# Optimization experiments

Hardware: AMD Instinct MI355X
Metric: run time of the kernel (lower is better)

## Reference

```python
import jax, jax.numpy as jnp
import numpy as np

B, D, H, O, E, TOP_K = 1024, 1024, 2048, 1024, 8, 2


def setup_inputs() -> dict:
    key = jax.random.key(0)
    ks = jax.random.split(key, 8)
    s = 0.02
    return {
        "x":  jax.random.normal(ks[0], (B, D), dtype=jnp.float32),
        "Wr": jax.random.normal(ks[1], (D, E), dtype=jnp.float32) * s,
        "br": jnp.zeros((E,), dtype=jnp.float32),
        "W1": jax.random.normal(ks[2], (E, D, H), dtype=jnp.float32) * s,
        "b1": jnp.zeros((E, H), dtype=jnp.float32),
        "W2": jax.random.normal(ks[3], (E, H, H), dtype=jnp.float32) * s,
        "b2": jnp.zeros((E, H), dtype=jnp.float32),
        "W3": jax.random.normal(ks[4], (E, H, O), dtype=jnp.float32) * s,
        "b3": jnp.zeros((E, O), dtype=jnp.float32),
    }


def reference(x, Wr, br, W1, b1, W2, b2, W3, b3):
    # --- router: softmax -> top-k -> renormalize selected weights ---
    logits = x @ Wr + br                      # [B, E]
    probs = jax.nn.softmax(logits, axis=-1)
    w, ids = jax.lax.top_k(probs, TOP_K)      # [B, K], [B, K]
    w = w / (jnp.sum(w, axis=-1, keepdims=True) + 1e-6)

    # --- expert MLPs (depth=2: in->h, relu, h->h, relu, h->out) ---
    h = jax.nn.relu(jnp.einsum('bd,edh->beh', x, W1) + b1)   # [B, E, H]
    h = jax.nn.relu(jnp.einsum('beh,ehg->beg', h, W2) + b2)  # [B, E, H]
    y_e = jnp.einsum('beg,ego->beo', h, W3) + b3             # [B, E, O]

    # --- weighted scatter-combine: comb[b,e] = sum_k w[b,k] * [ids[b,k]==e] ---
    comb = jnp.sum(jax.nn.one_hot(ids, E, dtype=x.dtype) * w[..., None], axis=1)  # [B, E]
    out = jnp.einsum('beo,be->bo', y_e, comb)                # [B, O]
    return out
```

## Files before the change

### kernel.cpp

```cpp
#include <hip/hip_runtime.h>
#include <hip/hip_bf16.h>

#define BT 1024
#define DD 1024
#define HH 2048
#define OO 1024
#define EE 8
#define RMAX 3072

typedef __bf16 bf16x8 __attribute__((ext_vector_type(8)));
typedef float  f32x4  __attribute__((ext_vector_type(4)));

__device__ __forceinline__ void cp16(void* l, const void* g) {
    __builtin_amdgcn_global_load_lds(
        (const __attribute__((address_space(1))) void*)g,
        (__attribute__((address_space(3))) void*)l, 16, 0, 0);
}


__global__ __launch_bounds__(256) void router_kernel(
    const float* __restrict__ x, const float* __restrict__ Wr, const float* __restrict__ br,
    int* __restrict__ counts, int* __restrict__ elist,
    int* __restrict__ tok_e, int* __restrict__ tok_p, float* __restrict__ tok_w)
{
    int b = blockIdx.x;
    int tid = threadIdx.x;
    float acc[EE];
#pragma unroll
    for (int e = 0; e < EE; ++e) acc[e] = 0.f;
    const float* xr = x + (size_t)b * DD;
    for (int d = tid; d < DD; d += 256) {
        float xv = xr[d];
#pragma unroll
        for (int e = 0; e < EE; ++e) acc[e] += xv * Wr[d * EE + e];
    }
    __shared__ float red[4][EE];
    int lane = tid & 63, wv = tid >> 6;
#pragma unroll
    for (int e = 0; e < EE; ++e) {
        float v = acc[e];
#pragma unroll
        for (int o = 32; o > 0; o >>= 1) v += __shfl_down(v, o, 64);
        if (lane == 0) red[wv][e] = v;
    }
    __syncthreads();
    if (tid == 0) {
        float lg[EE];
#pragma unroll
        for (int e = 0; e < EE; ++e) lg[e] = red[0][e] + red[1][e] + red[2][e] + red[3][e] + br[e];
        float mx = lg[0];
#pragma unroll
        for (int e = 1; e < EE; ++e) mx = fmaxf(mx, lg[e]);
        float s = 0.f, p[EE];
#pragma unroll
        for (int e = 0; e < EE; ++e) { p[e] = expf(lg[e] - mx); s += p[e]; }
        float inv = 1.f / s;
#pragma unroll
        for (int e = 0; e < EE; ++e) p[e] *= inv;
        int i0 = 0; float b0 = p[0];
#pragma unroll
        for (int e = 1; e < EE; ++e) if (p[e] > b0) { b0 = p[e]; i0 = e; }
        int i1 = -1; float b1v = -1.f;
#pragma unroll
        for (int e = 0; e < EE; ++e) if (e != i0 && p[e] > b1v) { b1v = p[e]; i1 = e; }
        float s2 = b0 + b1v + 1e-6f;
        float w0 = b0 / s2, w1 = b1v / s2;
        int p0 = atomicAdd(&counts[i0], 1);
        int p1 = atomicAdd(&counts[i1], 1);
        elist[i0 * 1024 + p0] = b;
        elist[i1 * 1024 + p1] = b;
        tok_e[2 * b] = i0; tok_e[2 * b + 1] = i1;
        tok_p[2 * b] = p0; tok_p[2 * b + 1] = p1;
        tok_w[2 * b] = w0; tok_w[2 * b + 1] = w1;
    }
}

__global__ void offsets_kernel(const int* __restrict__ counts, int* __restrict__ off)
{
    if (threadIdx.x == 0 && blockIdx.x == 0) {
        int a = 0;
        for (int e = 0; e < EE; ++e) {
            off[e] = a;
            a += ((counts[e] + 127) >> 7) << 7;
        }
        off[EE] = a;
    }
}

__global__ __launch_bounds__(256) void gather_kernel(
    const float* __restrict__ x, const int* __restrict__ counts, const int* __restrict__ off,
    const int* __restrict__ elist, __bf16* __restrict__ Xg)
{
    int e = blockIdx.y;
    int chunk = blockIdx.x >> 2;
    int rg = blockIdx.x & 3;
    int cnt = counts[e];
    if (chunk * 128 >= cnt) return;
    int base = off[e] + chunk * 128 + rg * 32;
    int tid = threadIdx.x;
    for (int it = 0; it < 32; ++it) {
        int slot = chunk * 128 + rg * 32 + it;
        __bf16 v[4];
        if (slot < cnt) {
            int tok = elist[e * 1024 + slot];
            const float4 f = *(const float4*)(x + (size_t)tok * DD + tid * 4);
            v[0] = (__bf16)f.x; v[1] = (__bf16)f.y; v[2] = (__bf16)f.z; v[3] = (__bf16)f.w;
        } else {
            v[0] = v[1] = v[2] = v[3] = (__bf16)0.f;
        }
        *(uint2*)(Xg + (size_t)(base + it) * DD + tid * 4) = *(uint2*)v;
    }
}

template <int K, int N, int TN, bool RELU, bool OUT_BF16>
__global__ __launch_bounds__(256) void gemm_fused(
    const __bf16* __restrict__ A, const float* __restrict__ Wall,
    const float* __restrict__ bias, void* __restrict__ OutV,
    const int* __restrict__ counts, const int* __restrict__ off)
{
    constexpr int NSTEPS = K / 32;
    constexpr int NJ  = TN / 32;
    constexpr int BLD = TN / 8;

    int e  = blockIdx.x & 7;
    int nt = blockIdx.x >> 3;
    int mt = blockIdx.y;
    int cnt = counts[e];
    if (mt * 128 >= cnt) return;
    int row0 = off[e] + mt * 128;

    const __bf16* Ab = A + (size_t)row0 * K;
    const float*  Wp = Wall + (size_t)e * K * N + nt * TN;

    __shared__ __bf16 As[2][128 * 32];
    __shared__ __bf16 Bs[2][TN * 40];

    int tid = threadIdx.x;
    int wave = tid >> 6, lane = tid & 63;
    int m = lane & 15, q = lane >> 4;
    int wm = (wave >> 1) * 64, wn = (wave & 1) * (TN / 2);

    int ar = wave * 16 + (lane >> 2);
    int k8 = (lane & 3) * 8;
    int bn  = (TN == 64) ? (tid & 63) : (tid & 31);
    int bkc = (TN == 64) ? ((tid >> 6) * 8) : ((tid >> 5) * 4);

    float breg[BLD];
    f32x4 acc[4][NJ] = {};

    auto issueA = [&](int t, int buf) {
        const __bf16* src = Ab + t * 32;
        cp16(&As[buf][ar * 32 + k8],        src + (size_t)ar * K + k8);
        cp16(&As[buf][(64 + ar) * 32 + k8], src + (size_t)(64 + ar) * K + k8);
    };
    auto loadB = [&](int t) {
        const float* p = Wp + (size_t)(t * 32 + bkc) * N + bn;
#pragma unroll
        for (int g = 0; g < BLD; ++g) breg[g] = p[(size_t)g * N];
    };
    auto writeB = [&](int buf) {
        __bf16 t8[BLD];
#pragma unroll
        for (int g = 0; g < BLD; ++g) t8[g] = (__bf16)breg[g];
        if constexpr (TN == 64) *(uint4*)(&Bs[buf][bn * 40 + bkc]) = *(uint4*)t8;
        else                    *(uint2*)(&Bs[buf][bn * 40 + bkc]) = *(uint2*)t8;
    };

    issueA(0, 0);
    loadB(0);
    __syncthreads();
    writeB(0);
    __syncthreads();

    for (int t = 0; t < NSTEPS; ++t) {
        int cur = t & 1;
        if (t + 1 < NSTEPS) {
            issueA(t + 1, cur ^ 1);
            loadB(t + 1);
        }
        bf16x8 af[4], bfr[NJ];
#pragma unroll
        for (int i = 0; i < 4; ++i)
            af[i] = *(bf16x8*)(&As[cur][(wm + i * 16 + m) * 32 + q * 8]);
#pragma unroll
        for (int j = 0; j < NJ; ++j)
            bfr[j] = *(bf16x8*)(&Bs[cur][(wn + j * 16 + m) * 40 + q * 8]);
#pragma unroll
        for (int i = 0; i < 4; ++i)
#pragma unroll
            for (int j = 0; j < NJ; ++j)
                acc[i][j] = __builtin_amdgcn_mfma_f32_16x16x32_bf16(af[i], bfr[j], acc[i][j], 0, 0, 0);
        if (t + 1 < NSTEPS) {
            __syncthreads();
            writeB(cur ^ 1);
            __syncthreads();
        }
    }

    const float* bp = bias + (size_t)e * N;
    int colbase = nt * TN + wn;
#pragma unroll
    for (int j = 0; j < NJ; ++j) {
        int col = colbase + j * 16 + m;
        float bv = bp[col];
#pragma unroll
        for (int i = 0; i < 4; ++i) {
            int rbase = row0 + wm + i * 16 + q * 4;
#pragma unroll
            for (int r = 0; r < 4; ++r) {
                float v = acc[i][j][r] + bv;
                if constexpr (RELU) v = fmaxf(v, 0.f);
                if constexpr (OUT_BF16)
                    ((__bf16*)OutV)[(size_t)(rbase + r) * N + col] = (__bf16)v;
                else
                    ((float*)OutV)[(size_t)(rbase + r) * N + col] = v;
            }
        }
    }
}

__global__ __launch_bounds__(256) void combine_kernel(
    const float* __restrict__ Y, const int* __restrict__ off,
    const int* __restrict__ tok_e, const int* __restrict__ tok_p,
    const float* __restrict__ tok_w, float* __restrict__ out)
{
    int b = blockIdx.x, t = threadIdx.x;
    int e0 = tok_e[2 * b], e1 = tok_e[2 * b + 1];
    int r0 = off[e0] + tok_p[2 * b];
    int r1 = off[e1] + tok_p[2 * b + 1];
    float w0 = tok_w[2 * b], w1 = tok_w[2 * b + 1];
    int col = t * 4;
    f32x4 s0 = *(const f32x4*)(Y + (size_t)r0 * OO + col);
    f32x4 s1 = *(const f32x4*)(Y + (size_t)r1 * OO + col);
    f32x4 o = s0 * w0 + s1 * w1;
    *(f32x4*)(out + (size_t)b * OO + col) = o;
}

extern "C" void kernel_launch(void* const* d_in, const int* in_sizes, int n_in,
                              void* d_out, int out_size, void* d_ws, size_t ws_size,
                              hipStream_t stream)
{
    (void)in_sizes; (void)n_in; (void)out_size; (void)ws_size;
    const float* x  = (const float*)d_in[0];
    const float* Wr = (const float*)d_in[1];
    const float* br = (const float*)d_in[2];
    const float* W1 = (const float*)d_in[3];
    const float* b1 = (const float*)d_in[4];
    const float* W2 = (const float*)d_in[5];
    const float* b2 = (const float*)d_in[6];
    const float* W3 = (const float*)d_in[7];
    const float* b3 = (const float*)d_in[8];
    float* out = (float*)d_out;

    char* ws = (char*)d_ws;
    int*    counts = (int*)(ws + 0);
    int*    off    = (int*)(ws + 256);
    int*    tok_e  = (int*)(ws + 1024);
    int*    tok_p  = (int*)(ws + 9216);
    float*  tok_w  = (float*)(ws + 17408);
    int*    elist  = (int*)(ws + 25600);
    __bf16* Xg     = (__bf16*)(ws + 65536);
    __bf16* H1     = (__bf16*)(ws + 6356992);
    __bf16* H2     = (__bf16*)(ws + 18939904);
    float*  Y      = (float*)(ws + 31522816);

    hipMemsetAsync(counts, 0, 256, stream);
    router_kernel<<<1024, 256, 0, stream>>>(x, Wr, br, counts, elist, tok_e, tok_p, tok_w);
    offsets_kernel<<<1, 64, 0, stream>>>(counts, off);
    gather_kernel<<<dim3(32, 8), 256, 0, stream>>>(x, counts, off, elist, Xg);

    gemm_fused<1024, 2048, 64, true,  true ><<<dim3(256, 8), 256, 0, stream>>>(Xg, W1, b1, (void*)H1, counts, off);
    gemm_fused<2048, 2048, 64, true,  true ><<<dim3(256, 8), 256, 0, stream>>>(H1, W2, b2, (void*)H2, counts, off);
    gemm_fused<2048, 1024, 32, false, false><<<dim3(256, 8), 256, 0, stream>>>(H2, W3, b3, (void*)Y,  counts, off);

    combine_kernel<<<1024, 256, 0, stream>>>(Y, off, tok_e, tok_p, tok_w, out);
}
```

Before: 439.5 us.

## Deepen MoE GEMM pipeline: K=64 steps, triple-buffered A, swizzled LDS, manual waitcnts

Rewrites the expert GEMM main loop to process 64-wide K steps with a three-stage A buffer filled by direct global-to-LDS loads and double-buffered fp32 B registers prefetched two steps ahead. LDS layouts switch from padded rows to XOR-swizzled rows to avoid bank conflicts. Explicit s_waitcnt, sched_barrier and setprio replace full __syncthreads pairs, so MFMA work can overlap outstanding loads, and launch bounds request two blocks per CU. The trade is more registers and LDS per block, plus fragile hand-tuned wait counts that could race if miscounted.

```diff
diff --git a/kernel.cpp b/kernel.cpp
--- a/kernel.cpp
+++ b/kernel.cpp
@@ -16,6 +16,11 @@
         (const __attribute__((address_space(1))) void*)g,
         (__attribute__((address_space(3))) void*)l, 16, 0, 0);
 }
+
+#define VMW(n)  asm volatile("s_waitcnt vmcnt(" #n ")" ::: "memory")
+#define LGKM(n) asm volatile("s_waitcnt lgkmcnt(" #n ")" ::: "memory")
+#define SCHED0  __builtin_amdgcn_sched_barrier(0)
+#define BAR()   __builtin_amdgcn_s_barrier()
 
 
 __global__ __launch_bounds__(256) void router_kernel(
@@ -113,14 +118,15 @@
 }
 
 template <int K, int N, int TN, bool RELU, bool OUT_BF16>
-__global__ __launch_bounds__(256) void gemm_fused(
+__global__ __launch_bounds__(256, 2) void gemm_fused(
     const __bf16* __restrict__ A, const float* __restrict__ Wall,
     const float* __restrict__ bias, void* __restrict__ OutV,
     const int* __restrict__ counts, const int* __restrict__ off)
 {
-    constexpr int NSTEPS = K / 32;
+    constexpr int NSTEPS = K / 64;
     constexpr int NJ  = TN / 32;
-    constexpr int BLD = TN / 8;
+    constexpr int BLD = TN / 4;
+    constexpr int BSE = TN * 64;
 
     int e  = blockIdx.x & 7;
     int nt = blockIdx.x >> 3;
@@ -132,69 +138,98 @@
     const __bf16* Ab = A + (size_t)row0 * K;
     const float*  Wp = Wall + (size_t)e * K * N + nt * TN;
 
-    __shared__ __bf16 As[2][128 * 32];
-    __shared__ __bf16 Bs[2][TN * 40];
+    __shared__ __bf16 As[3 * 8192];
+    __shared__ __bf16 Bs[2 * BSE];
 
     int tid = threadIdx.x;
     int wave = tid >> 6, lane = tid & 63;
     int m = lane & 15, q = lane >> 4;
     int wm = (wave >> 1) * 64, wn = (wave & 1) * (TN / 2);
 
-    int ar = wave * 16 + (lane >> 2);
-    int k8 = (lane & 3) * 8;
+    int rdma = wave * 8 + (lane >> 3);
+    int kxe  = ((lane & 7) ^ (lane >> 3)) * 8;
     int bn  = (TN == 64) ? (tid & 63) : (tid & 31);
-    int bkc = (TN == 64) ? ((tid >> 6) * 8) : ((tid >> 5) * 4);
-
-    float breg[BLD];
+    int bkc = (TN == 64) ? ((tid >> 6) * 16) : ((tid >> 5) * 8);
+    int c0  = bkc >> 3;
+    int bswz = bn & 7;
+
+    float bA[BLD], bB[BLD];
     f32x4 acc[4][NJ] = {};
 
-    auto issueA = [&](int t, int buf) {
-        const __bf16* src = Ab + t * 32;
-        cp16(&As[buf][ar * 32 + k8],        src + (size_t)ar * K + k8);
-        cp16(&As[buf][(64 + ar) * 32 + k8], src + (size_t)(64 + ar) * K + k8);
+    auto issueA = [&](int t, unsigned ab) {
+#pragma unroll
+        for (int i = 0; i < 4; ++i)
+            cp16(&As[ab + i * 2048 + wave * 512 + lane * 8],
+                 Ab + (size_t)(i * 32 + rdma) * K + t * 64 + kxe);
     };
-    auto loadB = [&](int t) {
-        const float* p = Wp + (size_t)(t * 32 + bkc) * N + bn;
-#pragma unroll
-        for (int g = 0; g < BLD; ++g) breg[g] = p[(size_t)g * N];
+    auto loadB = [&](int t, float (&br_)[BLD]) {
+        const float* p = Wp + (size_t)(t * 64 + bkc) * N + bn;
+#pragma unroll
+        for (int g = 0; g < BLD; ++g) br_[g] = p[(size_t)g * N];
     };
-    auto writeB = [&](int buf) {
+    auto writeB = [&](unsigned bb, float (&br_)[BLD]) {
         __bf16 t8[BLD];
 #pragma unroll
-        for (int g = 0; g < BLD; ++g) t8[g] = (__bf16)breg[g];
-        if constexpr (TN == 64) *(uint4*)(&Bs[buf][bn * 40 + bkc]) = *(uint4*)t8;
-        else                    *(uint2*)(&Bs[buf][bn * 40 + bkc]) = *(uint2*)t8;
+        for (int g = 0; g < BLD; ++g) t8[g] = (__bf16)br_[g];
+        *(uint4*)(&Bs[bb + bn * 64 + ((c0    ) ^ bswz) * 8]) = ((const uint4*)t8)[0];
+        if constexpr (TN == 64)
+            *(uint4*)(&Bs[bb + bn * 64 + ((c0 + 1) ^ bswz) * 8]) = ((const uint4*)t8)[1];
     };
 
-    issueA(0, 0);
-    loadB(0);
-    __syncthreads();
-    writeB(0);
-    __syncthreads();
-
-    for (int t = 0; t < NSTEPS; ++t) {
-        int cur = t & 1;
+    auto STEP = [&](int t, unsigned aR, unsigned aW, unsigned bR, unsigned bW,
+                    float (&bWr)[BLD], float (&bLd)[BLD]) {
+        BAR(); SCHED0;
+        bool pf = (t + 2 < NSTEPS);
+        if (pf) { issueA(t + 2, aW); loadB(t + 2, bLd); }
+        bf16x8 af[4][2], bfr[NJ][2];
+#pragma unroll
+        for (int kk = 0; kk < 2; ++kk) {
+#pragma unroll
+            for (int i = 0; i < 4; ++i)
+                af[i][kk] = *(bf16x8*)(&As[aR + (wm + i * 16 + m) * 64 + (((kk * 4 + q) ^ (m & 7)) * 8)]);
+#pragma unroll
+            for (int j = 0; j < NJ; ++j)
+                bfr[j][kk] = *(bf16x8*)(&Bs[bR + (wn + j * 16 + m) * 64 + (((kk * 4 + q) ^ (m & 7)) * 8)]);
+        }
+        if constexpr (NJ == 2) LGKM(6); else LGKM(5);
+        SCHED0;
+        __builtin_amdgcn_s_setprio(1);
+#pragma unroll
+        for (int i = 0; i < 4; ++i)
+#pragma unroll
+            for (int j = 0; j < NJ; ++j)
+                acc[i][j] = __builtin_amdgcn_mfma_f32_16x16x32_bf16(af[i][0], bfr[j][0], acc[i][j], 0, 0, 0);
+        LGKM(0); SCHED0;
+#pragma unroll
+        for (int i = 0; i < 4; ++i)
+#pragma unroll
+            for (int j = 0; j < NJ; ++j)
+                acc[i][j] = __builtin_amdgcn_mfma_f32_16x16x32_bf16(af[i][1], bfr[j][1], acc[i][j], 0, 0, 0);
+        __builtin_amdgcn_s_setprio(0);
         if (t + 1 < NSTEPS) {
-            issueA(t + 1, cur ^ 1);
-            loadB(t + 1);
-        }
-        bf16x8 af[4], bfr[NJ];
-#pragma unroll
-        for (int i = 0; i < 4; ++i)
-            af[i] = *(bf16x8*)(&As[cur][(wm + i * 16 + m) * 32 + q * 8]);
-#pragma unroll
-        for (int j = 0; j < NJ; ++j)
-            bfr[j] = *(bf16x8*)(&Bs[cur][(wn + j * 16 + m) * 40 + q * 8]);
-#pragma unroll
-        for (int i = 0; i < 4; ++i)
-#pragma unroll
-            for (int j = 0; j < NJ; ++j)
-                acc[i][j] = __builtin_amdgcn_mfma_f32_16x16x32_bf16(af[i], bfr[j], acc[i][j], 0, 0, 0);
-        if (t + 1 < NSTEPS) {
-            __syncthreads();
-            writeB(cur ^ 1);
-            __syncthreads();
-        }
+            if (pf) { if constexpr (TN == 64) VMW(20); else VMW(12); }
+            else    { VMW(0); }
+            SCHED0;
+            writeB(bW, bWr);
+            LGKM(0);
+        }
+    };
+
+    issueA(0, 0u);
+    issueA(1, 8192u);
+    loadB(0, bA);
+    loadB(1, bB);
+    if constexpr (TN == 64) VMW(16); else VMW(8);
+    SCHED0;
+    writeB(0u, bA);
+    LGKM(0);
+
+    unsigned aR = 0u, aM = 8192u, aW = 16384u;
+    for (int t = 0; t < NSTEPS; t += 2) {
+        STEP(t,     aR, aW, 0u,            (unsigned)BSE, bB, bA);
+        { unsigned tp = aR; aR = aM; aM = aW; aW = tp; }
+        STEP(t + 1, aR, aW, (unsigned)BSE, 0u,            bA, bB);
+        { unsigned tp = aR; aR = aM; aM = aW; aW = tp; }
     }
 
     const float* bp = bias + (size_t)e * N;
```

After: 433.0 us. About the same (-1.5%).
